# Kernel optimization log

Measured on AMD Instinct MI355X. Metric: run time of the kernel, lower is better.

The kernel has to match this reference:

```python
import jax, jax.numpy as jnp
import numpy as np

EPS = 1e-5

def ste(x):
    # straight-through sign: forward = sign(x), backward = identity
    # (matches torch .data mutation trick in BinarizeConv2d/BinarizeLinear)
    return x + jax.lax.stop_gradient(jnp.sign(x) - x)

def conv(x, w, stride, pad):
    return jax.lax.conv_general_dilated(
        x, w, window_strides=stride,
        padding=[(pad[0], pad[0]), (pad[1], pad[1])],
        dimension_numbers=('NCHW', 'OIHW', 'NCHW'))

def bn2d(x, g, b):  # training-mode batch stats (module default .train())
    m = jnp.mean(x, axis=(0, 2, 3), keepdims=True)
    v = jnp.var(x, axis=(0, 2, 3), keepdims=True)
    return (x - m) * jax.lax.rsqrt(v + EPS) * g[None, :, None, None] + b[None, :, None, None]

def bn1d(x, g, b):
    m = jnp.mean(x, axis=0, keepdims=True)
    v = jnp.var(x, axis=0, keepdims=True)
    return (x - m) * jax.lax.rsqrt(v + EPS) * g[None, :] + b[None, :]

def prelu(x, a):
    return jnp.where(x >= 0, x, a * x)

def _forward(x, w1, w2, w3, w4, w5, w6, w7, w8, w9, w10,
             g1, b1, g2, b2, g3, b3, g4, b4, g5, b5,
             a1, a2, a3, a4, a5,
             fc1, fc2, fc3, g6, b6, g7, b7, a6, a7):
    h = x[:, None]  # (B,1,1100,9)
    # stage cfg: (wa,wb), bn, prelu, pad_a, (stride_b), bin_input flags
    stages = [
        ((w1, w2), (g1, b1), a1, (2, 0), (5, 1), (False, False)),
        ((w3, w4), (g2, b2), a2, (2, 0), (5, 1), (True, True)),
        ((w5, w6), (g3, b3), a3, (5, 0), (11, 1), (True, True)),
        ((w7, w8), (g4, b4), a4, (0, 1), (1, 3), (True, True)),
        ((w9, w10), (g5, b5), a5, (0, 1), (1, 3), (True, True)),
    ]
    for (wa, wb), (g, b), a, pad_a, stride_b, (bin_a, bin_b) in stages:
        if bin_a:
            h = ste(h)
        h = conv(h, ste(wa), (1, 1), pad_a)
        if bin_b:
            h = ste(h)
        h = conv(h, ste(wb), stride_b, (0, 0))
        h = prelu(bn2d(h, g, b), a)
    h = h.reshape(h.shape[0], -1)  # (B,1024)
    h = h @ ste(fc1).T                       # no input binarization (flag False)
    h = prelu(bn1d(h, g6, b6), a6)           # dropout skipped (eval/deterministic)
    h = ste(h) @ ste(fc2).T
    h = prelu(bn1d(h, g7, b7), a7)
    h = ste(h) @ ste(fc3).T                  # (B,2)
    return h

def setup_inputs() -> dict:
    key = jax.random.key(0)
    ks = jax.random.split(key, 20)
    C = [16, 32, 64, 128, 256]
    width = 0.01
    d = {'x': jax.random.normal(ks[0], (512, 1100, 9), jnp.float32)}
    shapes = [
        (C[0], 1, 5, 1), (C[0], C[0], 5, 1),
        (C[1], C[0], 5, 1), (C[1], C[1], 5, 1),
        (C[2], C[1], 11, 1), (C[2], C[2], 11, 1),
        (C[3], C[2], 1, 3), (C[3], C[3], 1, 3),
        (C[4], C[3], 1, 3), (C[4], C[4], 1, 3),
    ]
    for i, s in enumerate(shapes):
        d[f'w{i+1}'] = jax.random.normal(ks[1 + i], s, jnp.float32) * width
    for i, c in enumerate(C):
        d[f'g{i+1}'] = jnp.ones((c,), jnp.float32)
        d[f'b{i+1}'] = jnp.zeros((c,), jnp.float32)
        d[f'a{i+1}'] = jnp.asarray(0.25, jnp.float32)
    d['fc1'] = jax.random.uniform(ks[11], (256, 1024), jnp.float32, -width / 2, width / 2)
    d['fc2'] = jax.random.uniform(ks[12], (64, 256), jnp.float32, -width / 2, width / 2)
    d['fc3'] = jax.random.uniform(ks[13], (2, 64), jnp.float32, -width / 2, width / 2)
    d['g6'] = jnp.ones((256,), jnp.float32); d['b6'] = jnp.zeros((256,), jnp.float32)
    d['g7'] = jnp.ones((64,), jnp.float32); d['b7'] = jnp.zeros((64,), jnp.float32)
    d['a6'] = jnp.asarray(0.25, jnp.float32); d['a7'] = jnp.asarray(0.25, jnp.float32)
    return d

def reference(x, w1, w2, w3, w4, w5, w6, w7, w8, w9, w10,
              g1, b1, g2, b2, g3, b3, g4, b4, g5, b5,
              a1, a2, a3, a4, a5,
              fc1, fc2, fc3, g6, b6, g7, b7, a6, a7):
    return _forward(x, w1, w2, w3, w4, w5, w6, w7, w8, w9, w10,
                    g1, b1, g2, b2, g3, b3, g4, b4, g5, b5,
                    a1, a2, a3, a4, a5,
                    fc1, fc2, fc3, g6, b6, g7, b7, a6, a7)
```

## Files before the change

kernel.cpp:

```cpp
#include <hip/hip_runtime.h>
#include <hip/hip_bf16.h>

#define EPSV 1e-5

__device__ __forceinline__ float fsign(float x) {
    return (float)((x > 0.f) - (x < 0.f));
}

struct WPtrs {
    const float* src[3];
    float* dst[3];
    int n[3];
};

__global__ void sign_weights_kernel(WPtrs wp) {
    int wi = blockIdx.y;
    int n = wp.n[wi];
    const float* s = wp.src[wi];
    float* d = wp.dst[wi];
    for (int i = blockIdx.x * blockDim.x + threadIdx.x; i < n; i += gridDim.x * blockDim.x)
        d[i] = fsign(s[i]);
}

__global__ void build_wc_kernel(const float* __restrict__ w1, const float* __restrict__ w2,
                                float* __restrict__ wc) {
    int t = threadIdx.x;
    if (t < 208) {
        int co = t / 13, r = t % 13;
        float s = 0.f;
        for (int ci = 0; ci < 16; ++ci)
#pragma unroll
            for (int kh = 0; kh < 5; ++kh) {
                int k5 = r - kh;
                if (k5 >= 0 && k5 < 5)
                    s += fsign(w2[(co * 16 + ci) * 5 + kh]) * fsign(w1[ci * 5 + k5]);
            }
        wc[t] = s;
    }
}

struct PW { const float* src; unsigned* dnz; unsigned* dsg; int cout, cin, k, nw; };
struct PWall { PW l[8]; };

__global__ void pack_weights_kernel(PWall pa) {
    PW p = pa.l[blockIdx.y];
    int total = p.cout * p.k * p.nw;
    for (int u = blockIdx.x * blockDim.x + threadIdx.x; u < total; u += gridDim.x * blockDim.x) {
        int co = u / (p.k * p.nw);
        int rem = u % (p.k * p.nw);
        int kk = rem / p.nw, wi = rem % p.nw;
        unsigned nz = 0, sg = 0;
        for (int j = 0; j < 32; ++j) {
            int ci = wi * 32 + j;
            if (ci < p.cin) {
                float v = p.src[(co * p.cin + ci) * p.k + kk];
                if (v != 0.f) nz |= 1u << j;
                if (v < 0.f) sg |= 1u << j;
            }
        }
        p.dnz[u] = nz;
        p.dsg[u] = sg;
    }
}

__global__ void stats_finalp(const double* __restrict__ part, int S, long count,
                             float* __restrict__ mean, float* __restrict__ rstd) {
    int c = blockIdx.x, t = threadIdx.x;
    int chunk = (S + 255) / 256;
    int lo = t * chunk, hi = min(S, lo + chunk);
    double s = 0, q = 0;
    for (int i = lo; i < hi; ++i) {
        s += part[((long)c * S + i) * 2];
        q += part[((long)c * S + i) * 2 + 1];
    }
    __shared__ double ls[256], lq[256];
    ls[t] = s; lq[t] = q;
    __syncthreads();
    for (int off = 128; off > 0; off >>= 1) {
        if (t < off) { ls[t] += ls[t + off]; lq[t] += lq[t + off]; }
        __syncthreads();
    }
    if (t == 0) {
        double m = ls[0] / (double)count;
        double v = lq[0] / (double)count - m * m;
        mean[c] = (float)m;
        rstd[c] = (float)(1.0 / sqrt(v + EPSV));
    }
}

__global__ void stats_bn1d(const float* __restrict__ x, int C, int N,
                           float* __restrict__ mean, float* __restrict__ rstd) {
    int c = blockIdx.x;
    double sum = 0, sq = 0;
    for (int n = threadIdx.x; n < N; n += 64) {
        float v = x[(long)n * C + c];
        sum += v;
        sq += (double)v * v;
    }
    for (int off = 32; off > 0; off >>= 1) {
        sum += __shfl_down(sum, off);
        sq += __shfl_down(sq, off);
    }
    if (threadIdx.x == 0) {
        double m = sum / (double)N;
        double v = sq / (double)N - m * m;
        mean[c] = (float)m;
        rstd[c] = (float)(1.0 / sqrt(v + EPSV));
    }
}

__global__ void stage1_kernel(const float* __restrict__ x, const float* __restrict__ wcg,
                              float* __restrict__ p1, double* __restrict__ part) {
    int n = blockIdx.y;
    int hb = blockIdx.x;
    int ho0 = hb * 28;
    int nrows = min(28, 220 - ho0);
    int nrx = 5 * nrows + 8;
    __shared__ float xs[148 * 9];
    __shared__ float wcl[208];
    __shared__ float st[252 * 17];
    __shared__ double sS[16 * 16], sQ[16 * 16];
    int t = threadIdx.x;
    if (t < 208) wcl[t] = wcg[t];
    int hbase = 5 * ho0 - 2;
    for (int i = t; i < nrx * 9; i += 256) {
        int r = i / 9, w = i - r * 9, h = hbase + r;
        xs[i] = (h >= 0 && h < 1100) ? x[(n * 1100 + h) * 9 + w] : 0.f;
    }
    __syncthreads();
    int npos = nrows * 9;
    if (t < npos) {
        int hoL = t / 9, w = t - hoL * 9;
        double xr[13];
        int base = 45 * hoL + w;
#pragma unroll
        for (int r = 0; r < 13; ++r) xr[r] = (double)xs[base + 9 * r];
#pragma unroll
        for (int co = 0; co < 16; ++co) {
            double acc = 0.0;
#pragma unroll
            for (int r = 0; r < 13; ++r)
                acc += (double)wcl[co * 13 + r] * xr[r];
            st[t * 17 + co] = (float)acc;
        }
    }
    __syncthreads();
    float4* dst = (float4*)(p1 + (((long)n * 1980 + ho0 * 9) << 4));
    int nf4 = npos * 4;
    for (int u = t; u < nf4; u += 256) {
        int pos = u >> 2, q4 = (u & 3) << 2;
        const float* s4 = &st[pos * 17 + q4];
        dst[u] = make_float4(s4[0], s4[1], s4[2], s4[3]);
    }
    {
        int co = t & 15, seg = t >> 4;
        double s = 0, q = 0;
        for (int pos = seg; pos < npos; pos += 16) {
            double v = (double)st[pos * 17 + co];
            s += v; q += v * v;
        }
        sS[seg * 16 + co] = s;
        sQ[seg * 16 + co] = q;
    }
    __syncthreads();
    if (t < 16) {
        double s = 0, q = 0;
#pragma unroll
        for (int seg = 0; seg < 16; ++seg) {
            s += sS[seg * 16 + t];
            q += sQ[seg * 16 + t];
        }
        long blk = (long)n * 8 + hb;
        part[((long)t * 4096 + blk) * 2] = s;
        part[((long)t * 4096 + blk) * 2 + 1] = q;
    }
}

__global__ void stage2_kernel(const float* __restrict__ p1, const float* __restrict__ mean,
    const float* __restrict__ rstd, const float* __restrict__ g, const float* __restrict__ b,
    const float* __restrict__ ap, const unsigned* __restrict__ w3n, const unsigned* __restrict__ w3s,
    const unsigned* __restrict__ w4n, const unsigned* __restrict__ w4s, float* __restrict__ p2,
    double* __restrict__ part) {
    int hb = blockIdx.x;
    int n = blockIdx.y;
    float a = ap[0];
    __shared__ __align__(16) uint2 qx[216];
    __shared__ __align__(16) uint2 ax[180];
    __shared__ __align__(16) uint2 w3L[160];
    __shared__ __align__(16) uint2 w4L[160];
    __shared__ float sArr[1152];
    int t = threadIdx.x;
    if (t < 160) {
        int kh = t / 32, co = t % 32;
        w3L[t] = make_uint2(w3n[co * 5 + kh], w3s[co * 5 + kh]);
        w4L[t] = make_uint2(w4n[t], w4s[t]);
    }
    if (t < 216) {
        int rl = t / 9, w = t % 9;
        int r = 20 * hb - 2 + rl;
        unsigned nz = 0, sg = 0;
        if (r >= 0 && r < 220) {
            const float4* src = (const float4*)(p1 + (((long)n * 1980 + r * 9 + w) << 4));
            float4 v4[4];
#pragma unroll
            for (int q4 = 0; q4 < 4; ++q4) v4[q4] = src[q4];
            const float* vals = (const float*)v4;
#pragma unroll
            for (int ci = 0; ci < 16; ++ci) {
                float bnv = (vals[ci] - mean[ci]) * rstd[ci] * g[ci] + b[ci];
                float pr = bnv < 0.f ? a * bnv : bnv;
                if (pr != 0.f) { nz |= 1u << ci; if (pr < 0.f) sg |= 1u << ci; }
            }
        }
        qx[t] = make_uint2(nz, sg);
    }
    __syncthreads();
    if (t < 180) {
        int jl = t / 9, w = t % 9;
        uint2 xv[5];
#pragma unroll
        for (int kh = 0; kh < 5; ++kh) xv[kh] = qx[(jl + kh) * 9 + w];
        unsigned onz = 0, osg = 0;
        for (int co = 0; co < 32; co += 2) {
            int c0 = 0, n0 = 0, c1 = 0, n1 = 0;
#pragma unroll
            for (int kh = 0; kh < 5; ++kh) {
                const uint4 wv = *(const uint4*)&w3L[kh * 32 + co];
                unsigned b0 = xv[kh].x & wv.x;
                c0 += __popc(b0);
                n0 += __popc((xv[kh].y ^ wv.y) & b0);
                unsigned b1 = xv[kh].x & wv.z;
                c1 += __popc(b1);
                n1 += __popc((xv[kh].y ^ wv.w) & b1);
            }
            int s0 = c0 - 2 * n0, s1 = c1 - 2 * n1;
            if (s0 != 0) { onz |= 1u << co; if (s0 < 0) osg |= 1u << co; }
            if (s1 != 0) { onz |= 1u << (co + 1); if (s1 < 0) osg |= 1u << (co + 1); }
        }
        ax[t] = make_uint2(onz, osg);
    }
    __syncthreads();
    for (int o = t; o < 1152; o += 256) {
        int pos = o >> 5, co = o & 31;
        int hol = pos / 9, w = pos % 9;
        int cnt = 0, neg = 0;
#pragma unroll
        for (int kh = 0; kh < 5; ++kh) {
            uint2 av = ax[(5 * hol + kh) * 9 + w];
            uint2 wv = w4L[co * 5 + kh];
            unsigned both = av.x & wv.x;
            cnt += __popc(both);
            neg += __popc((av.y ^ wv.y) & both);
        }
        float val = (float)(cnt - 2 * neg);
        sArr[o] = val;
        p2[(((long)n * 396 + (4 * hb + hol) * 9 + w) << 5) + co] = val;
    }
    __syncthreads();
    if (t < 32) {
        double s = 0, q = 0;
        for (int pos = 0; pos < 36; ++pos) {
            double v = (double)sArr[pos * 32 + t];
            s += v; q += v * v;
        }
        long blk = (long)hb * 512 + n;
        part[((long)t * 5632 + blk) * 2] = s;
        part[((long)t * 5632 + blk) * 2 + 1] = q;
    }
}

__global__ void stage3_kernel(const float* __restrict__ p2, const float* __restrict__ mean,
    const float* __restrict__ rstd, const float* __restrict__ g, const float* __restrict__ b,
    const float* __restrict__ ap, const unsigned* __restrict__ w5n, const unsigned* __restrict__ w5s,
    const unsigned* __restrict__ w6n, const unsigned* __restrict__ w6s, float* __restrict__ p3,
    double* __restrict__ part) {
    int ho = blockIdx.x;
    int n = blockIdx.y;
    float a = ap[0];
    __shared__ __align__(16) uint2 qx[189];
    __shared__ __align__(16) uint2 ax[99 * 2];
    __shared__ __align__(16) uint2 w5L[704];
    __shared__ __align__(16) uint2 w6L[1408];
    __shared__ float sArr[576];
    int t = threadIdx.x;
    for (int i = t; i < 704; i += 256) {
        int kh = i / 64, co = i % 64;
        w5L[i] = make_uint2(w5n[co * 11 + kh], w5s[co * 11 + kh]);
    }
    for (int i = t; i < 1408; i += 256)
        w6L[i] = make_uint2(w6n[i], w6s[i]);
    if (t < 189) {
        int rl = t / 9, w = t % 9;
        int r = 11 * ho - 5 + rl;
        unsigned nz = 0, sg = 0;
        if (r >= 0 && r < 44) {
            const float4* src = (const float4*)(p2 + (((long)n * 396 + r * 9 + w) << 5));
            float4 v4[8];
#pragma unroll
            for (int q4 = 0; q4 < 8; ++q4) v4[q4] = src[q4];
            const float* vals = (const float*)v4;
#pragma unroll
            for (int ci = 0; ci < 32; ++ci) {
                float bnv = (vals[ci] - mean[ci]) * rstd[ci] * g[ci] + b[ci];
                float pr = bnv < 0.f ? a * bnv : bnv;
                if (pr != 0.f) { nz |= 1u << ci; if (pr < 0.f) sg |= 1u << ci; }
            }
        }
        qx[t] = make_uint2(nz, sg);
    }
    __syncthreads();
    if (t < 198) {
        int p = t >> 1, wi = t & 1;
        int jl = p / 9, w = p % 9;
        uint2 xv[11];
#pragma unroll
        for (int kh = 0; kh < 11; ++kh) xv[kh] = qx[(jl + kh) * 9 + w];
        unsigned onz = 0, osg = 0;
        for (int jj = 0; jj < 32; jj += 2) {
            int co0 = wi * 32 + jj;
            int c0 = 0, n0 = 0, c1 = 0, n1 = 0;
#pragma unroll
            for (int kh = 0; kh < 11; ++kh) {
                const uint4 wv = *(const uint4*)&w5L[kh * 64 + co0];
                unsigned b0 = xv[kh].x & wv.x;
                c0 += __popc(b0);
                n0 += __popc((xv[kh].y ^ wv.y) & b0);
                unsigned b1 = xv[kh].x & wv.z;
                c1 += __popc(b1);
                n1 += __popc((xv[kh].y ^ wv.w) & b1);
            }
            int s0 = c0 - 2 * n0, s1 = c1 - 2 * n1;
            if (s0 != 0) { onz |= 1u << jj; if (s0 < 0) osg |= 1u << jj; }
            if (s1 != 0) { onz |= 1u << (jj + 1); if (s1 < 0) osg |= 1u << (jj + 1); }
        }
        ax[p * 2 + wi] = make_uint2(onz, osg);
    }
    __syncthreads();
    for (int o = t; o < 576; o += 256) {
        int co = o & 63, w = o >> 6;
        int cA = 0, nA = 0, cB = 0, nB = 0;
        for (int kh = 0; kh < 11; ++kh) {
            const uint4 av = *(const uint4*)&ax[(kh * 9 + w) * 2];
            const uint4 wv = *(const uint4*)&w6L[(co * 11 + kh) * 2];
            unsigned b0 = av.x & wv.x;
            cA += __popc(b0);
            nA += __popc((av.y ^ wv.y) & b0);
            unsigned b1 = av.z & wv.z;
            cB += __popc(b1);
            nB += __popc((av.w ^ wv.w) & b1);
        }
        float val = (float)((cA + cB) - 2 * (nA + nB));
        sArr[o] = val;
        p3[(((long)n * 36 + ho * 9 + w) << 6) + co] = val;
    }
    __syncthreads();
    if (t < 64) {
        double s = 0, q = 0;
        for (int w = 0; w < 9; ++w) {
            double v = (double)sArr[w * 64 + t];
            s += v; q += v * v;
        }
        long blk = (long)ho * 512 + n;
        part[((long)t * 2048 + blk) * 2] = s;
        part[((long)t * 2048 + blk) * 2 + 1] = q;
    }
}

__global__ void stage4_kernel(const float* __restrict__ p3, const float* __restrict__ mean,
    const float* __restrict__ rstd, const float* __restrict__ g, const float* __restrict__ b,
    const float* __restrict__ ap, const unsigned* __restrict__ w7n, const unsigned* __restrict__ w7s,
    const unsigned* __restrict__ w8n, const unsigned* __restrict__ w8s, float* __restrict__ p4,
    double* __restrict__ part) {
    int h = blockIdx.x;
    int n = blockIdx.y;
    float a = ap[0];
    __shared__ unsigned q[9 * 4];
    __shared__ signed char strit[9 * 128];
    __shared__ unsigned an[9 * 4], ag[9 * 4];
    __shared__ float sArr[384];
    int t = threadIdx.x;
    if (t < 18) {
        int w = t >> 1, half = t & 1;
        const float4* src = (const float4*)(p3 + (((long)n * 36 + h * 9 + w) << 6) + half * 32);
        float4 v4[8];
#pragma unroll
        for (int q4 = 0; q4 < 8; ++q4) v4[q4] = src[q4];
        const float* vals = (const float*)v4;
        unsigned nz = 0, sg = 0;
#pragma unroll
        for (int j = 0; j < 32; ++j) {
            int ci = half * 32 + j;
            float bnv = (vals[j] - mean[ci]) * rstd[ci] * g[ci] + b[ci];
            float pr = bnv < 0.f ? a * bnv : bnv;
            if (pr != 0.f) { nz |= 1u << j; if (pr < 0.f) sg |= 1u << j; }
        }
        q[w * 4 + half] = nz; q[w * 4 + 2 + half] = sg;
    }
    __syncthreads();
    for (int o = t; o < 1152; o += 256) {
        int w = o / 128, co = o % 128;
        int cnt = 0, neg = 0;
        for (int kw = 0; kw < 3; ++kw) {
            int wl = w + kw - 1;
            if (wl < 0 || wl >= 9) continue;
#pragma unroll
            for (int iw = 0; iw < 2; ++iw) {
                unsigned both = q[wl * 4 + iw] & w7n[(co * 3 + kw) * 2 + iw];
                cnt += __popc(both);
                neg += __popc((q[wl * 4 + 2 + iw] ^ w7s[(co * 3 + kw) * 2 + iw]) & both);
            }
        }
        int s = cnt - 2 * neg;
        strit[o] = (signed char)((s > 0) - (s < 0));
    }
    __syncthreads();
    if (t < 36) {
        int w = t >> 2, wi = t & 3;
        unsigned nz = 0, sg = 0;
        for (int j = 0; j < 32; ++j) {
            int tr = strit[w * 128 + wi * 32 + j];
            if (tr) { nz |= 1u << j; if (tr < 0) sg |= 1u << j; }
        }
        an[w * 4 + wi] = nz; ag[w * 4 + wi] = sg;
    }
    __syncthreads();
    for (int o = t; o < 384; o += 256) {
        int wo = o >> 7, co = o & 127;
        int cnt = 0, neg = 0;
        for (int kw = 0; kw < 3; ++kw) {
            int wl = 3 * wo + kw;
#pragma unroll
            for (int iw = 0; iw < 4; ++iw) {
                unsigned both = an[wl * 4 + iw] & w8n[(co * 3 + kw) * 4 + iw];
                cnt += __popc(both);
                neg += __popc((ag[wl * 4 + iw] ^ w8s[(co * 3 + kw) * 4 + iw]) & both);
            }
        }
        float val = (float)(cnt - 2 * neg);
        sArr[o] = val;
        p4[(((long)n * 12 + h * 3 + wo) << 7) + co] = val;
    }
    __syncthreads();
    if (t < 128) {
        double s = 0, qd = 0;
        for (int wo = 0; wo < 3; ++wo) {
            double v = (double)sArr[wo * 128 + t];
            s += v; qd += v * v;
        }
        long blk = (long)h * 512 + n;
        part[((long)t * 2048 + blk) * 2] = s;
        part[((long)t * 2048 + blk) * 2 + 1] = qd;
    }
}

__global__ void stage5_kernel(const float* __restrict__ p4, const float* __restrict__ mean,
    const float* __restrict__ rstd, const float* __restrict__ g, const float* __restrict__ b,
    const float* __restrict__ ap, const unsigned* __restrict__ w9n, const unsigned* __restrict__ w9s,
    const unsigned* __restrict__ w10n, const unsigned* __restrict__ w10s, float* __restrict__ p5,
    double* __restrict__ part) {
    int h = blockIdx.x;
    int n = blockIdx.y;
    float a = ap[0];
    __shared__ unsigned q[3 * 8];
    __shared__ signed char strit[3 * 256];
    __shared__ unsigned an[3 * 8], ag[3 * 8];
    int t = threadIdx.x;
    if (t < 12) {
        int w = t >> 2, wq = t & 3;
        const float4* src = (const float4*)(p4 + (((long)n * 12 + h * 3 + w) << 7) + wq * 32);
        float4 v4[8];
#pragma unroll
        for (int q4 = 0; q4 < 8; ++q4) v4[q4] = src[q4];
        const float* vals = (const float*)v4;
        unsigned nz = 0, sg = 0;
#pragma unroll
        for (int j = 0; j < 32; ++j) {
            int ci = wq * 32 + j;
            float bnv = (vals[j] - mean[ci]) * rstd[ci] * g[ci] + b[ci];
            float pr = bnv < 0.f ? a * bnv : bnv;
            if (pr != 0.f) { nz |= 1u << j; if (pr < 0.f) sg |= 1u << j; }
        }
        q[w * 8 + wq] = nz; q[w * 8 + 4 + wq] = sg;
    }
    __syncthreads();
    for (int o = t; o < 768; o += 256) {
        int w = o / 256, co = o % 256;
        int cnt = 0, neg = 0;
        for (int kw = 0; kw < 3; ++kw) {
            int wl = w + kw - 1;
            if (wl < 0 || wl >= 3) continue;
#pragma unroll
            for (int iw = 0; iw < 4; ++iw) {
                unsigned both = q[wl * 8 + iw] & w9n[(co * 3 + kw) * 4 + iw];
                cnt += __popc(both);
                neg += __popc((q[wl * 8 + 4 + iw] ^ w9s[(co * 3 + kw) * 4 + iw]) & both);
            }
        }
        int s = cnt - 2 * neg;
        strit[o] = (signed char)((s > 0) - (s < 0));
    }
    __syncthreads();
    if (t < 24) {
        int w = t >> 3, wi = t & 7;
        unsigned nz = 0, sg = 0;
        for (int j = 0; j < 32; ++j) {
            int tr = strit[w * 256 + wi * 32 + j];
            if (tr) { nz |= 1u << j; if (tr < 0) sg |= 1u << j; }
        }
        an[w * 8 + wi] = nz; ag[w * 8 + wi] = sg;
    }
    __syncthreads();
    if (t < 256) {
        int co = t;
        int cnt = 0, neg = 0;
        for (int kw = 0; kw < 3; ++kw) {
#pragma unroll
            for (int iw = 0; iw < 8; ++iw) {
                unsigned both = an[kw * 8 + iw] & w10n[(co * 3 + kw) * 8 + iw];
                cnt += __popc(both);
                neg += __popc((ag[kw * 8 + iw] ^ w10s[(co * 3 + kw) * 8 + iw]) & both);
            }
        }
        float val = (float)(cnt - 2 * neg);
        p5[(long)n * 1024 + co * 4 + h] = val;
        long blk = (long)h * 512 + n;
        double v = (double)val;
        part[((long)co * 2048 + blk) * 2] = v;
        part[((long)co * 2048 + blk) * 2 + 1] = v * v;
    }
}

__global__ void fc1_kernel(const float* __restrict__ p5, const float* __restrict__ mean,
                           const float* __restrict__ rstd, const float* __restrict__ g,
                           const float* __restrict__ b, const float* __restrict__ ap,
                           const float* __restrict__ sfc1, float* __restrict__ h1) {
    int n = blockIdx.x;
    float a = ap[0];
    __shared__ float hv[1024];
    int t = threadIdx.x;
    for (int idx = t; idx < 1024; idx += 256) {
        int c = idx >> 2;
        float v = p5[n * 1024 + idx];
        float bnv = (v - mean[c]) * rstd[c] * g[c] + b[c];
        hv[idx] = bnv < 0.f ? a * bnv : bnv;
    }
    __syncthreads();
    int wave = t >> 6, lane = t & 63;
    float hr[16];
#pragma unroll
    for (int m = 0; m < 16; ++m) hr[m] = hv[lane * 16 + m];
    for (int jj = 0; jj < 64; ++jj) {
        int j = wave * 64 + jj;
        const float4* wr = (const float4*)(sfc1 + (j << 10) + (lane << 4));
        double s = 0.0;
#pragma unroll
        for (int q4 = 0; q4 < 4; ++q4) {
            float4 wv = wr[q4];
            s += (double)(hr[q4 * 4 + 0] * wv.x);
            s += (double)(hr[q4 * 4 + 1] * wv.y);
            s += (double)(hr[q4 * 4 + 2] * wv.z);
            s += (double)(hr[q4 * 4 + 3] * wv.w);
        }
#pragma unroll
        for (int off = 32; off > 0; off >>= 1) s += __shfl_down(s, off, 64);
        if (lane == 0) h1[n * 256 + j] = (float)s;
    }
}

__global__ void fc2_kernel(const float* __restrict__ h1, const float* __restrict__ mean,
                           const float* __restrict__ rstd, const float* __restrict__ g,
                           const float* __restrict__ b, const float* __restrict__ ap,
                           const float* __restrict__ sfc2, float* __restrict__ h2) {
    int n = blockIdx.x;
    float a = ap[0];
    __shared__ float sv[256];
    int t = threadIdx.x;
    if (t < 256) {
        float v = h1[n * 256 + t];
        float bnv = (v - mean[t]) * rstd[t] * g[t] + b[t];
        float pr = bnv < 0.f ? a * bnv : bnv;
        sv[t] = fsign(pr);
    }
    __syncthreads();
    if (t < 64) {
        float s = 0.f;
        for (int k = 0; k < 256; ++k) s += sv[k] * sfc2[t * 256 + k];
        h2[n * 64 + t] = s;
    }
}

__global__ void fc3_kernel(const float* __restrict__ h2, const float* __restrict__ mean,
                           const float* __restrict__ rstd, const float* __restrict__ g,
                           const float* __restrict__ b, const float* __restrict__ ap,
                           const float* __restrict__ sfc3, float* __restrict__ out) {
    int n = blockIdx.x;
    float a = ap[0];
    __shared__ float sv[64];
    int t = threadIdx.x;
    if (t < 64) {
        float v = h2[n * 64 + t];
        float bnv = (v - mean[t]) * rstd[t] * g[t] + b[t];
        float pr = bnv < 0.f ? a * bnv : bnv;
        sv[t] = fsign(pr);
    }
    __syncthreads();
    if (t < 2) {
        float s = 0.f;
        for (int k = 0; k < 64; ++k) s += sv[k] * sfc3[t * 64 + k];
        out[n * 2 + t] = s;
    }
}

extern "C" void kernel_launch(void* const* d_in, const int* in_sizes, int n_in,
                              void* d_out, int out_size, void* d_ws, size_t ws_size,
                              hipStream_t stream) {
    const float* x = (const float*)d_in[0];
    const float* G[8] = {nullptr, (const float*)d_in[11], (const float*)d_in[14],
                         (const float*)d_in[17], (const float*)d_in[20], (const float*)d_in[23],
                         (const float*)d_in[29], (const float*)d_in[31]};
    const float* B[8] = {nullptr, (const float*)d_in[12], (const float*)d_in[15],
                         (const float*)d_in[18], (const float*)d_in[21], (const float*)d_in[24],
                         (const float*)d_in[30], (const float*)d_in[32]};
    const float* A[8] = {nullptr, (const float*)d_in[13], (const float*)d_in[16],
                         (const float*)d_in[19], (const float*)d_in[22], (const float*)d_in[25],
                         (const float*)d_in[33], (const float*)d_in[34]};

    float* ws = (float*)d_ws;
    size_t off = 0;
    const int fsz[3] = {262144, 16384, 128};
    float* fw[3];
    for (int i = 0; i < 3; ++i) { fw[i] = ws + off; off += (size_t)fsz[i]; }
    float* sfc1 = fw[0]; float* sfc2 = fw[1]; float* sfc3 = fw[2];
    float* wc = ws + off; off += 208;

    const int psz[8] = {160, 160, 704, 1408, 768, 1536, 3072, 6144};
    unsigned* pn[8]; unsigned* pg[8];
    for (int i = 0; i < 8; ++i) {
        pn[i] = (unsigned*)(ws + off); off += (size_t)psz[i];
        pg[i] = (unsigned*)(ws + off); off += (size_t)psz[i];
    }

    float* p1 = ws + off; off += 16220160;
    float* p2 = ws + off; off += 6488064;
    float* p3 = ws + off; off += 1179648;
    float* p4 = ws + off; off += 786432;
    float* p5 = ws + off; off += 524288;
    float* h1 = ws + off; off += 131072;
    float* h2 = ws + off; off += 32768;
    float* mean1 = ws + off; off += 16;  float* rstd1 = ws + off; off += 16;
    float* mean2 = ws + off; off += 32;  float* rstd2 = ws + off; off += 32;
    float* mean3 = ws + off; off += 64;  float* rstd3 = ws + off; off += 64;
    float* mean4 = ws + off; off += 128; float* rstd4 = ws + off; off += 128;
    float* mean5 = ws + off; off += 256; float* rstd5 = ws + off; off += 256;
    float* mean6 = ws + off; off += 256; float* rstd6 = ws + off; off += 256;
    float* mean7 = ws + off; off += 64;  float* rstd7 = ws + off; off += 64;
    if (off & 1) off += 1;
    double* part = (double*)(ws + off); off += 2 * 1048576;

    WPtrs wp;
    const int fsrc_idx[3] = {26, 27, 28};
    for (int i = 0; i < 3; ++i) {
        wp.src[i] = (const float*)d_in[fsrc_idx[i]];
        wp.dst[i] = fw[i];
        wp.n[i] = fsz[i];
    }
    hipLaunchKernelGGL(sign_weights_kernel, dim3(32, 3), dim3(256), 0, stream, wp);
    hipLaunchKernelGGL(build_wc_kernel, dim3(1), dim3(256), 0, stream,
                       (const float*)d_in[1], (const float*)d_in[2], wc);

    PWall pa;
    const int cout_[8] = {32, 32, 64, 64, 128, 128, 256, 256};
    const int cin_[8]  = {16, 32, 32, 64, 64, 128, 128, 256};
    const int kk_[8]   = {5, 5, 11, 11, 3, 3, 3, 3};
    for (int i = 0; i < 8; ++i) {
        pa.l[i].src = (const float*)d_in[3 + i];
        pa.l[i].dnz = pn[i];
        pa.l[i].dsg = pg[i];
        pa.l[i].cout = cout_[i];
        pa.l[i].cin = cin_[i];
        pa.l[i].k = kk_[i];
        pa.l[i].nw = (cin_[i] + 31) / 32;
    }
    hipLaunchKernelGGL(pack_weights_kernel, dim3(4, 8), dim3(256), 0, stream, pa);

    hipLaunchKernelGGL(stage1_kernel, dim3(8, 512), dim3(256), 0, stream, x, wc, p1, part);
    hipLaunchKernelGGL(stats_finalp, dim3(16), dim3(256), 0, stream, part, 4096,
                       (long)512 * 1980, mean1, rstd1);

    hipLaunchKernelGGL(stage2_kernel, dim3(11, 512), dim3(256), 0, stream, p1, mean1, rstd1,
                       G[1], B[1], A[1], pn[0], pg[0], pn[1], pg[1], p2, part);
    hipLaunchKernelGGL(stats_finalp, dim3(32), dim3(256), 0, stream, part, 5632,
                       (long)512 * 396, mean2, rstd2);

    hipLaunchKernelGGL(stage3_kernel, dim3(4, 512), dim3(256), 0, stream, p2, mean2, rstd2,
                       G[2], B[2], A[2], pn[2], pg[2], pn[3], pg[3], p3, part);
    hipLaunchKernelGGL(stats_finalp, dim3(64), dim3(256), 0, stream, part, 2048,
                       (long)512 * 36, mean3, rstd3);

    hipLaunchKernelGGL(stage4_kernel, dim3(4, 512), dim3(256), 0, stream, p3, mean3, rstd3,
                       G[3], B[3], A[3], pn[4], pg[4], pn[5], pg[5], p4, part);
    hipLaunchKernelGGL(stats_finalp, dim3(128), dim3(256), 0, stream, part, 2048,
                       (long)512 * 12, mean4, rstd4);

    hipLaunchKernelGGL(stage5_kernel, dim3(4, 512), dim3(256), 0, stream, p4, mean4, rstd4,
                       G[4], B[4], A[4], pn[6], pg[6], pn[7], pg[7], p5, part);
    hipLaunchKernelGGL(stats_finalp, dim3(256), dim3(256), 0, stream, part, 2048,
                       (long)512 * 4, mean5, rstd5);

    hipLaunchKernelGGL(fc1_kernel, dim3(512), dim3(256), 0, stream, p5, mean5, rstd5,
                       G[5], B[5], A[5], sfc1, h1);
    hipLaunchKernelGGL(stats_bn1d, dim3(256), dim3(64), 0, stream, h1, 256, 512, mean6, rstd6);

    hipLaunchKernelGGL(fc2_kernel, dim3(512), dim3(256), 0, stream, h1, mean6, rstd6,
                       G[6], B[6], A[6], sfc2, h2);
    hipLaunchKernelGGL(stats_bn1d, dim3(64), dim3(64), 0, stream, h2, 64, 512, mean7, rstd7);

    hipLaunchKernelGGL(fc3_kernel, dim3(512), dim3(256), 0, stream, h2, mean7, rstd7,
                       G[7], B[7], A[7], sfc3, (float*)d_out);
}
```

Baseline: 299.5 us.

## Register-block first binary conv over 4 output rows and transpose second-conv weights in LDS

In stages 2 and 3, each thread of the first (kh-tap) binary convolution now computes 4 consecutive output rows and keeps a sliding window of input rows in registers, so each weight vector read from LDS is reused 4 times. The second-conv weights are rearranged in LDS to kh-major order so consecutive threads (consecutive co) read adjacent entries, which avoids bank conflicts. The cost is that far fewer threads are active in the first conv phase (45 and 54 instead of 180 and 198), so that phase runs with less parallelism and more registers per thread.

Result: slower. 339.0 us (median of 2 runs) (+13.2%).

```diff
diff --git a/kernel.cpp b/kernel.cpp
--- a/kernel.cpp
+++ b/kernel.cpp
@@ -193,7 +193,7 @@
     if (t < 160) {
         int kh = t / 32, co = t % 32;
         w3L[t] = make_uint2(w3n[co * 5 + kh], w3s[co * 5 + kh]);
-        w4L[t] = make_uint2(w4n[t], w4s[t]);
+        w4L[t] = make_uint2(w4n[co * 5 + kh], w4s[co * 5 + kh]);
     }
     if (t < 216) {
         int rl = t / 9, w = t % 9;
@@ -215,29 +215,39 @@
         qx[t] = make_uint2(nz, sg);
     }
     __syncthreads();
-    if (t < 180) {
-        int jl = t / 9, w = t % 9;
-        uint2 xv[5];
-#pragma unroll
-        for (int kh = 0; kh < 5; ++kh) xv[kh] = qx[(jl + kh) * 9 + w];
-        unsigned onz = 0, osg = 0;
+    if (t < 45) {
+        int rp = t / 9, w = t % 9;
+        int jl0 = rp * 4;
+        uint2 xw[8];
+#pragma unroll
+        for (int r = 0; r < 8; ++r) xw[r] = qx[(jl0 + r) * 9 + w];
+        unsigned onz[4] = {0, 0, 0, 0}, osg[4] = {0, 0, 0, 0};
         for (int co = 0; co < 32; co += 2) {
-            int c0 = 0, n0 = 0, c1 = 0, n1 = 0;
+            int c0[4] = {0, 0, 0, 0}, n0[4] = {0, 0, 0, 0};
+            int c1[4] = {0, 0, 0, 0}, n1[4] = {0, 0, 0, 0};
 #pragma unroll
             for (int kh = 0; kh < 5; ++kh) {
                 const uint4 wv = *(const uint4*)&w3L[kh * 32 + co];
-                unsigned b0 = xv[kh].x & wv.x;
-                c0 += __popc(b0);
-                n0 += __popc((xv[kh].y ^ wv.y) & b0);
-                unsigned b1 = xv[kh].x & wv.z;
-                c1 += __popc(b1);
-                n1 += __popc((xv[kh].y ^ wv.w) & b1);
-            }
-            int s0 = c0 - 2 * n0, s1 = c1 - 2 * n1;
-            if (s0 != 0) { onz |= 1u << co; if (s0 < 0) osg |= 1u << co; }
-            if (s1 != 0) { onz |= 1u << (co + 1); if (s1 < 0) osg |= 1u << (co + 1); }
-        }
-        ax[t] = make_uint2(onz, osg);
+#pragma unroll
+                for (int r = 0; r < 4; ++r) {
+                    unsigned b0 = xw[r + kh].x & wv.x;
+                    c0[r] += __popc(b0);
+                    n0[r] += __popc((xw[r + kh].y ^ wv.y) & b0);
+                    unsigned b1 = xw[r + kh].x & wv.z;
+                    c1[r] += __popc(b1);
+                    n1[r] += __popc((xw[r + kh].y ^ wv.w) & b1);
+                }
+            }
+#pragma unroll
+            for (int r = 0; r < 4; ++r) {
+                int s0 = c0[r] - 2 * n0[r], s1 = c1[r] - 2 * n1[r];
+                if (s0 != 0) { onz[r] |= 1u << co; if (s0 < 0) osg[r] |= 1u << co; }
+                if (s1 != 0) { onz[r] |= 1u << (co + 1); if (s1 < 0) osg[r] |= 1u << (co + 1); }
+            }
+        }
+#pragma unroll
+        for (int r = 0; r < 4; ++r)
+            ax[(jl0 + r) * 9 + w] = make_uint2(onz[r], osg[r]);
     }
     __syncthreads();
     for (int o = t; o < 1152; o += 256) {
@@ -247,7 +257,7 @@
 #pragma unroll
         for (int kh = 0; kh < 5; ++kh) {
             uint2 av = ax[(5 * hol + kh) * 9 + w];
-            uint2 wv = w4L[co * 5 + kh];
+            uint2 wv = w4L[kh * 32 + co];
             unsigned both = av.x & wv.x;
             cnt += __popc(both);
             neg += __popc((av.y ^ wv.y) & both);
@@ -287,8 +297,11 @@
         int kh = i / 64, co = i % 64;
         w5L[i] = make_uint2(w5n[co * 11 + kh], w5s[co * 11 + kh]);
     }
-    for (int i = t; i < 1408; i += 256)
-        w6L[i] = make_uint2(w6n[i], w6s[i]);
+    for (int i = t; i < 1408; i += 256) {
+        int pair = i >> 1, wi = i & 1;
+        int kh = pair / 64, co = pair % 64;
+        w6L[i] = make_uint2(w6n[(co * 11 + kh) * 2 + wi], w6s[(co * 11 + kh) * 2 + wi]);
+    }
     if (t < 189) {
         int rl = t / 9, w = t % 9;
         int r = 11 * ho - 5 + rl;
@@ -309,31 +322,44 @@
         qx[t] = make_uint2(nz, sg);
     }
     __syncthreads();
-    if (t < 198) {
-        int p = t >> 1, wi = t & 1;
-        int jl = p / 9, w = p % 9;
-        uint2 xv[11];
-#pragma unroll
-        for (int kh = 0; kh < 11; ++kh) xv[kh] = qx[(jl + kh) * 9 + w];
-        unsigned onz = 0, osg = 0;
+    if (t < 54) {
+        int u = t >> 1, wi = t & 1;
+        int rp = u / 9, w = u % 9;
+        int jl0 = rp * 4;
+        int nv = (rp < 2) ? 4 : 3;
+        uint2 xw[14];
+#pragma unroll
+        for (int r = 0; r < 14; ++r) {
+            int row = jl0 + r;
+            xw[r] = (row < 21) ? qx[row * 9 + w] : make_uint2(0u, 0u);
+        }
+        unsigned onz[4] = {0, 0, 0, 0}, osg[4] = {0, 0, 0, 0};
         for (int jj = 0; jj < 32; jj += 2) {
             int co0 = wi * 32 + jj;
-            int c0 = 0, n0 = 0, c1 = 0, n1 = 0;
+            int c0[4] = {0, 0, 0, 0}, n0[4] = {0, 0, 0, 0};
+            int c1[4] = {0, 0, 0, 0}, n1[4] = {0, 0, 0, 0};
 #pragma unroll
             for (int kh = 0; kh < 11; ++kh) {
                 const uint4 wv = *(const uint4*)&w5L[kh * 64 + co0];
-                unsigned b0 = xv[kh].x & wv.x;
-                c0 += __popc(b0);
-                n0 += __popc((xv[kh].y ^ wv.y) & b0);
-                unsigned b1 = xv[kh].x & wv.z;
-                c1 += __popc(b1);
-                n1 += __popc((xv[kh].y ^ wv.w) & b1);
-            }
-            int s0 = c0 - 2 * n0, s1 = c1 - 2 * n1;
-            if (s0 != 0) { onz |= 1u << jj; if (s0 < 0) osg |= 1u << jj; }
-            if (s1 != 0) { onz |= 1u << (jj + 1); if (s1 < 0) osg |= 1u << (jj + 1); }
-        }
-        ax[p * 2 + wi] = make_uint2(onz, osg);
+#pragma unroll
+                for (int r = 0; r < 4; ++r) {
+                    unsigned b0 = xw[r + kh].x & wv.x;
+                    c0[r] += __popc(b0);
+                    n0[r] += __popc((xw[r + kh].y ^ wv.y) & b0);
+                    unsigned b1 = xw[r + kh].x & wv.z;
+                    c1[r] += __popc(b1);
+                    n1[r] += __popc((xw[r + kh].y ^ wv.w) & b1);
+                }
+            }
+#pragma unroll
+            for (int r = 0; r < 4; ++r) {
+                int s0 = c0[r] - 2 * n0[r], s1 = c1[r] - 2 * n1[r];
+                if (s0 != 0) { onz[r] |= 1u << jj; if (s0 < 0) osg[r] |= 1u << jj; }
+                if (s1 != 0) { onz[r] |= 1u << (jj + 1); if (s1 < 0) osg[r] |= 1u << (jj + 1); }
+            }
+        }
+        for (int r = 0; r < nv; ++r)
+            ax[((jl0 + r) * 9 + w) * 2 + wi] = make_uint2(onz[r], osg[r]);
     }
     __syncthreads();
     for (int o = t; o < 576; o += 256) {
@@ -341,7 +367,7 @@
         int cA = 0, nA = 0, cB = 0, nB = 0;
         for (int kh = 0; kh < 11; ++kh) {
             const uint4 av = *(const uint4*)&ax[(kh * 9 + w) * 2];
-            const uint4 wv = *(const uint4*)&w6L[(co * 11 + kh) * 2];
+            const uint4 wv = *(const uint4*)&w6L[(kh * 64 + co) * 2];
             unsigned b0 = av.x & wv.x;
             cA += __popc(b0);
             nA += __popc((av.y ^ wv.y) & b0);
```
